# Performance work log

Hardware: AMD Instinct MI355X
Metric: run time of the kernel (lower is better)

The kernel has to match this reference:

```python
import jax, jax.numpy as jnp
import numpy as np

HEADS = 4
DIM_HEAD = 64
SCALE = 10.0
EPS = 1e-12  # matches torch F.normalize default eps


def setup_inputs() -> dict:
    key = jax.random.key(0)
    k1, k2, k3, k4, k5 = jax.random.split(key, 5)
    dim = 256
    hidden = HEADS * DIM_HEAD
    x = jax.random.normal(k1, (16, dim, 32, 32), dtype=jnp.float32)
    y = jax.random.normal(k2, (16, dim, 32, 32), dtype=jnp.float32)
    # 1x1 conv weights stored as 2D matrices (out_ch, in_ch)
    w_qkv = jax.random.normal(k3, (hidden * 3, dim), dtype=jnp.float32) * (1.0 / np.sqrt(dim))
    w_out = jax.random.normal(k4, (dim, hidden), dtype=jnp.float32) * (1.0 / np.sqrt(hidden))
    b_out = jax.random.normal(k5, (dim,), dtype=jnp.float32) * 0.01
    return {"x": x, "y": y, "w_qkv": w_qkv, "w_out": w_out, "b_out": b_out}


def _l2norm(t):
    # torch F.normalize(t, dim=-1): t / max(||t||_2, eps)
    n = jnp.sqrt(jnp.sum(t * t, axis=-1, keepdims=True))
    return t / jnp.maximum(n, EPS)


def reference(x, y, w_qkv, w_out, b_out):
    b, c, hh, ww = x.shape
    n_x = hh * ww
    n_y = y.shape[2] * y.shape[3]
    hidden = HEADS * DIM_HEAD

    # 1x1 convs == channel matmuls; only q from x and k,v from y are used
    w_q, w_k, w_v = w_qkv[:hidden], w_qkv[hidden:2 * hidden], w_qkv[2 * hidden:]
    q = jnp.einsum('oc,bcn->bon', w_q, x.reshape(b, c, n_x)).reshape(b, HEADS, DIM_HEAD, n_x)
    k = jnp.einsum('oc,bcn->bon', w_k, y.reshape(b, c, n_y)).reshape(b, HEADS, DIM_HEAD, n_y)
    v = jnp.einsum('oc,bcn->bon', w_v, y.reshape(b, c, n_y)).reshape(b, HEADS, DIM_HEAD, n_y)

    # l2norm over the spatial (last) axis, as in the source
    q = _l2norm(q)
    k = _l2norm(k)

    sim = jnp.einsum('bhdi,bhdj->bhij', q, k) * SCALE          # [b,h,n_x,n_y]
    attn = jax.nn.softmax(sim, axis=-1)
    out = jnp.einsum('bhij,bhdj->bhid', attn, v)                # [b,h,n_x,d]

    # 'b h (x y) d -> b (h d) x y'
    out = out.transpose(0, 1, 3, 2).reshape(b, hidden, hh, ww)
    out = jnp.einsum('oc,bcn->bon', w_out, out.reshape(b, hidden, n_x))
    out = out + b_out[None, :, None]
    return out.reshape(b, -1, hh, ww)
```

## Files before the change

### kernel.cpp

```cpp
#include <hip/hip_runtime.h>
#include <hip/hip_bf16.h>
#include <stdint.h>

typedef __attribute__((ext_vector_type(8))) short short8;
typedef __attribute__((ext_vector_type(4))) float f32x4;

#define MFMA16(a, b, c) __builtin_amdgcn_mfma_f32_16x16x32_bf16((a), (b), (c), 0, 0, 0)


__device__ __forceinline__ ushort f2bf(float f) {
  union { float f; unsigned u; } x; x.f = f;
  unsigned r = x.u + 0x7FFFu + ((x.u >> 16) & 1u);
  return (ushort)(r >> 16);
}

__device__ __forceinline__ float bf2f(ushort u) {
  union { unsigned u; float f; } x; x.u = ((unsigned)u) << 16;
  return x.f;
}

__device__ __forceinline__ short8 ld8(const ushort* p) {
  return *reinterpret_cast<const short8*>(p);
}

__device__ __forceinline__ void gll16(const void* g, void* l) {
  __builtin_amdgcn_global_load_lds(
      reinterpret_cast<const __attribute__((address_space(1))) unsigned int*>(
          reinterpret_cast<uintptr_t>(g)),
      reinterpret_cast<__attribute__((address_space(3))) unsigned int*>(
          reinterpret_cast<uintptr_t>(l)),
      16, 0, 0);
}

__global__ __launch_bounds__(256) void k_tcvt(const float* __restrict__ x,
    const float* __restrict__ y, ushort* __restrict__ xbt, ushort* __restrict__ ybt) {
  int tile = blockIdx.x;
  const float* src; ushort* dst;
  if (tile >= 1024) { tile -= 1024; src = y; dst = ybt; }
  else { src = x; dst = xbt; }
  int b = tile >> 6;
  int c0 = ((tile >> 4) & 3) << 6;
  int n0 = (tile & 15) << 6;
  __shared__ ushort lds[64][65];
  int tid = threadIdx.x;
  int nl = tid & 63, cl = tid >> 6;
  const float* sb = src + ((size_t)b << 18);
#pragma unroll
  for (int s = 0; s < 16; ++s) {
    int c = cl + (s << 2);
    lds[c][nl] = f2bf(sb[(size_t)(c0 + c) * 1024 + n0 + nl]);
  }
  __syncthreads();
  ushort* db = dst + ((size_t)b << 18);
  int cl2 = tid & 63, nl2 = tid >> 6;
#pragma unroll
  for (int s = 0; s < 16; ++s) {
    int n = nl2 + (s << 2);
    db[(size_t)(n0 + n) * 256 + c0 + cl2] = lds[cl2][n];
  }
}

__global__ __launch_bounds__(256) void k_wcvt(const float* __restrict__ wqkv,
    const float* __restrict__ wout, ushort* __restrict__ wqkvb, ushort* __restrict__ woutb) {
  const int total1 = 768 * 256;
  const int total = total1 + 256 * 256;
  for (int i = blockIdx.x * 256 + threadIdx.x; i < total; i += gridDim.x * 256) {
    if (i < total1) wqkvb[i] = f2bf(wqkv[i]);
    else woutb[i - total1] = f2bf(wout[i - total1]);
  }
}

__global__ __launch_bounds__(512, 6) void k_qkv(const ushort* __restrict__ wqkvb,
    const ushort* __restrict__ xbt, const ushort* __restrict__ ybt,
    ushort* __restrict__ qraw, ushort* __restrict__ kraw,
    ushort* __restrict__ vbuf, float* __restrict__ norms2) {
  int bid = blockIdx.x;
  int lid = (bid & 7) * 96 + (bid >> 3);
  int ox = lid % 24;
  int t = lid / 24;
  int nb = t & 1;
  int b = t >> 1;
  int o0 = ox * 32;
  const ushort* Bsrc = (o0 < 256) ? xbt : ybt;
  const ushort* Bm = Bsrc + ((size_t)b << 18);
  int tid = threadIdx.x;
  int l = tid & 63, w = tid >> 6;
  int r = l & 15, g = l >> 4;
  const ushort* Ab = wqkvb + (size_t)(o0 + r) * 256 + g * 8;
  const ushort* Bb = Bm + (size_t)(nb * 512 + w * 64 + r) * 256 + g * 8;
  f32x4 acc[2][4];
#pragma unroll
  for (int i = 0; i < 2; ++i)
#pragma unroll
    for (int j = 0; j < 4; ++j) acc[i][j] = (f32x4){0.f, 0.f, 0.f, 0.f};
#pragma unroll
  for (int ks = 0; ks < 8; ++ks) {
    short8 a0 = ld8(Ab + ks * 32);
    short8 a1 = ld8(Ab + 4096 + ks * 32);
#pragma unroll
    for (int nf = 0; nf < 4; ++nf) {
      short8 bv = ld8(Bb + (size_t)nf * 4096 + ks * 32);
      acc[0][nf] = MFMA16(a0, bv, acc[0][nf]);
      acc[1][nf] = MFMA16(a1, bv, acc[1][nf]);
    }
  }
  __shared__ float snorm[8][32];
  if (o0 < 512) {
    float ss[2][4];
#pragma unroll
    for (int mf = 0; mf < 2; ++mf)
#pragma unroll
      for (int reg = 0; reg < 4; ++reg) {
        float s = 0.f;
#pragma unroll
        for (int nf = 0; nf < 4; ++nf) { float v = acc[mf][nf][reg]; s += v * v; }
#pragma unroll
        for (int m = 1; m < 16; m <<= 1) s += __shfl_xor(s, m);
        ss[mf][reg] = s;
      }
    if (r == 0) {
#pragma unroll
      for (int mf = 0; mf < 2; ++mf)
#pragma unroll
        for (int reg = 0; reg < 4; ++reg)
          snorm[w][mf * 16 + g * 4 + reg] = ss[mf][reg];
    }
    __syncthreads();
    if (tid < 32) {
      float s = 0.f;
#pragma unroll
      for (int w2 = 0; w2 < 8; ++w2) s += snorm[w2][tid];
      norms2[(nb * 16 + b) * 512 + o0 + tid] = s;
    }
  }
#pragma unroll
  for (int mf = 0; mf < 2; ++mf) {
    int ob = o0 + mf * 16 + g * 4;
#pragma unroll
    for (int nf = 0; nf < 4; ++nf) {
      int n = nb * 512 + w * 64 + nf * 16 + r;
#pragma unroll
      for (int reg = 0; reg < 4; ++reg) {
        ushort v = f2bf(acc[mf][nf][reg]);
        int oo = ob + reg;
        if (o0 < 256)       qraw[(((size_t)b * 256 + oo) << 10) + n] = v;
        else if (o0 < 512)  kraw[(((size_t)b * 256 + (oo - 256)) << 10) + n] = v;
        else                vbuf[(((size_t)b * 256 + (oo - 512)) << 10) + n] = v;
      }
    }
  }
}

__global__ __launch_bounds__(256) void k_normt(const ushort* __restrict__ qraw,
    const ushort* __restrict__ kraw, const float* __restrict__ norms2,
    ushort* __restrict__ qt, ushort* __restrict__ kt) {
  int tile = blockIdx.x;
  const ushort* src; ushort* dst; int which;
  if (tile >= 1024) { tile -= 1024; src = kraw; dst = kt; which = 1; }
  else { src = qraw; dst = qt; which = 0; }
  int b = tile >> 6;
  int h = (tile >> 4) & 3;
  int n0 = (tile & 15) << 6;
  __shared__ ushort lds[64][65];
  __shared__ float fs[64];
  int tid = threadIdx.x;
  if (tid < 64) {
    int idx = b * 512 + which * 256 + h * 64 + tid;
    float ss = norms2[idx] + norms2[8192 + idx];
    fs[tid] = (which ? 1.0f : 10.0f) / fmaxf(sqrtf(ss), 1e-12f);
  }
  __syncthreads();
  const ushort* sb = src + (((size_t)b * 256 + h * 64) << 10);
  int nl = tid & 63, dl = tid >> 6;
#pragma unroll
  for (int s = 0; s < 16; ++s) {
    int d = dl + (s << 2);
    lds[d][nl] = f2bf(bf2f(sb[((size_t)d << 10) + n0 + nl]) * fs[d]);
  }
  __syncthreads();
  ushort* db = dst + (((size_t)(b * 4 + h) << 10) + n0) * 64;
  int dl2 = tid & 63, nl2 = tid >> 6;
#pragma unroll
  for (int s = 0; s < 16; ++s) {
    int n = nl2 + (s << 2);
    db[(size_t)n * 64 + dl2] = lds[dl2][n];
  }
}

__global__ __launch_bounds__(512, 2) void k_attn(const ushort* __restrict__ qt,
    const ushort* __restrict__ kt, const ushort* __restrict__ vbuf,
    ushort* __restrict__ aot) {
  int hb = blockIdx.x;
  int it = blockIdx.y;
  int h = hb & 3, b = hb >> 2;
  int tid = threadIdx.x;
  int l = tid & 63, w = tid >> 6;
  int r = l & 15, g = l >> 4;
  size_t ho = ((size_t)hb) << 16;
  const ushort* Q = qt + ho;
  const char* Kg = (const char*)(kt + ho);
  const char* Vg = (const char*)(vbuf + ((size_t)b << 18) + ((size_t)h << 16));
  int i0 = it * 256 + w * 32;

  __shared__ __align__(16) ushort Kb[2][4096];
  __shared__ __align__(16) ushort Vb[2][4096];
  __shared__ __align__(16) ushort plds[8][2048];

  int L = w * 1024 + l * 16;
  int srow = L >> 7;
  int swz = (srow & 7) << 4;
  int ksrc = L ^ swz;
  int vsrc_col = (L & 127) ^ swz;

  short8 qa[2][2];
#pragma unroll
  for (int mf = 0; mf < 2; ++mf)
#pragma unroll
    for (int ks = 0; ks < 2; ++ks)
      qa[mf][ks] = ld8(Q + (size_t)(i0 + mf * 16 + r) * 64 + ks * 32 + g * 8);

  f32x4 oacc[2][4];
  float rsum[2][4];
#pragma unroll
  for (int mf = 0; mf < 2; ++mf)
#pragma unroll
    for (int j = 0; j < 4; ++j) { oacc[mf][j] = (f32x4){0.f, 0.f, 0.f, 0.f}; rsum[mf][j] = 0.f; }

#define STAGE(buf, j0v) do { \
    gll16(Kg + (j0v) * 128 + ksrc, (char*)&Kb[buf][0] + w * 1024); \
    gll16(Vg + (size_t)srow * 2048 + (j0v) * 2 + vsrc_col, (char*)&Vb[buf][0] + w * 1024); \
  } while (0)

  STAGE(0, 0);
  __syncthreads();

  char* plc = (char*)plds[w];
  for (int t = 0; t < 16; ++t) {
    int cur = t & 1;
    if (t < 15) STAGE(cur ^ 1, (t + 1) * 64);
    const char* Kc = (const char*)&Kb[cur][0];
    const char* Vc = (const char*)&Vb[cur][0];
    f32x4 sacc[2][4];
#pragma unroll
    for (int mf = 0; mf < 2; ++mf)
#pragma unroll
      for (int nf = 0; nf < 4; ++nf) sacc[mf][nf] = (f32x4){0.f, 0.f, 0.f, 0.f};
#pragma unroll
    for (int nf = 0; nf < 4; ++nf) {
      int row = nf * 16 + r;
      int sw = (row & 7) << 4;
      short8 k0 = *reinterpret_cast<const short8*>(Kc + ((row * 128 + g * 16) ^ sw));
      short8 k1 = *reinterpret_cast<const short8*>(Kc + ((row * 128 + 64 + g * 16) ^ sw));
      sacc[0][nf] = MFMA16(qa[0][0], k0, sacc[0][nf]);
      sacc[0][nf] = MFMA16(qa[0][1], k1, sacc[0][nf]);
      sacc[1][nf] = MFMA16(qa[1][0], k0, sacc[1][nf]);
      sacc[1][nf] = MFMA16(qa[1][1], k1, sacc[1][nf]);
    }
#pragma unroll
    for (int mf = 0; mf < 2; ++mf)
#pragma unroll
      for (int nf = 0; nf < 4; ++nf)
#pragma unroll
        for (int reg = 0; reg < 4; ++reg) {
          float p = __expf(sacc[mf][nf][reg]);
          rsum[mf][reg] += p;
          union { float f; unsigned u; } cv; cv.f = p;
          int row = mf * 16 + g * 4 + reg;
          int xorv = ((row ^ (row >> 3)) & 7) << 4;
          int byteo = row * 128 + (((nf * 16 + r) * 2) ^ xorv);
          *(ushort*)(plc + byteo) = (ushort)(cv.u >> 16);
        }
    short8 pa[2][2];
#pragma unroll
    for (int mf = 0; mf < 2; ++mf)
#pragma unroll
      for (int ks = 0; ks < 2; ++ks) {
        int row = mf * 16 + r;
        int xorv = (row ^ (row >> 3)) & 7;
        int blk = (ks * 4 + g) ^ xorv;
        pa[mf][ks] = *reinterpret_cast<const short8*>(plc + row * 128 + blk * 16);
      }
#pragma unroll
    for (int df = 0; df < 4; ++df) {
      int row = df * 16 + r;
      int sw = (row & 7) << 4;
#pragma unroll
      for (int ks = 0; ks < 2; ++ks) {
        short8 vf = *reinterpret_cast<const short8*>(Vc + ((row * 128 + ks * 64 + g * 16) ^ sw));
        oacc[0][df] = MFMA16(pa[0][ks], vf, oacc[0][df]);
        oacc[1][df] = MFMA16(pa[1][ks], vf, oacc[1][df]);
      }
    }
    __syncthreads();
  }
#undef STAGE

#pragma unroll
  for (int mf = 0; mf < 2; ++mf)
#pragma unroll
    for (int reg = 0; reg < 4; ++reg) {
      float s = rsum[mf][reg];
#pragma unroll
      for (int m = 1; m < 16; m <<= 1) s += __shfl_xor(s, m);
      rsum[mf][reg] = 1.0f / s;
    }
#pragma unroll
  for (int mf = 0; mf < 2; ++mf)
#pragma unroll
    for (int df = 0; df < 4; ++df)
#pragma unroll
      for (int reg = 0; reg < 4; ++reg) {
        int i = i0 + mf * 16 + g * 4 + reg;
        int d = df * 16 + r;
        float vo = oacc[mf][df][reg] * rsum[mf][reg];
        aot[((size_t)b << 18) + (size_t)i * 256 + h * 64 + d] = f2bf(vo);
      }
}

__global__ __launch_bounds__(512, 6) void k_out(const ushort* __restrict__ woutb,
    const ushort* __restrict__ aot, const float* __restrict__ bout,
    float* __restrict__ out) {
  int bid = blockIdx.x;
  int lid = (bid & 7) * 64 + (bid >> 3);
  int ox = lid & 15;
  int t = lid >> 4;
  int nb = t & 1;
  int b = t >> 1;
  int o0 = ox * 16;
  int tid = threadIdx.x, l = tid & 63, w = tid >> 6, r = l & 15, g = l >> 4;
  const ushort* Ab = woutb + (size_t)(o0 + r) * 256 + g * 8;
  const ushort* Bb = aot + ((size_t)b << 18) + (size_t)(nb * 512 + w * 64 + r) * 256 + g * 8;
  f32x4 acc[4];
#pragma unroll
  for (int j = 0; j < 4; ++j) acc[j] = (f32x4){0.f, 0.f, 0.f, 0.f};
#pragma unroll
  for (int ks = 0; ks < 8; ++ks) {
    short8 a0 = ld8(Ab + ks * 32);
#pragma unroll
    for (int nf = 0; nf < 4; ++nf) {
      short8 bv = ld8(Bb + (size_t)nf * 4096 + ks * 32);
      acc[nf] = MFMA16(a0, bv, acc[nf]);
    }
  }
  float bias[4];
#pragma unroll
  for (int reg = 0; reg < 4; ++reg) bias[reg] = bout[o0 + g * 4 + reg];
#pragma unroll
  for (int nf = 0; nf < 4; ++nf)
#pragma unroll
    for (int reg = 0; reg < 4; ++reg) {
      size_t o = (size_t)(b * 256 + o0 + g * 4 + reg);
      out[(o << 10) + nb * 512 + w * 64 + nf * 16 + r] = acc[nf][reg] + bias[reg];
    }
}

extern "C" void kernel_launch(void* const* d_in, const int* in_sizes, int n_in,
                              void* d_out, int out_size, void* d_ws, size_t ws_size,
                              hipStream_t stream) {
  const float* x     = (const float*)d_in[0];
  const float* y     = (const float*)d_in[1];
  const float* wqkv  = (const float*)d_in[2];
  const float* wout  = (const float*)d_in[3];
  const float* bout  = (const float*)d_in[4];
  float* out = (float*)d_out;
  char* ws = (char*)d_ws;

  ushort* xbt   = (ushort*)(ws + 0ull);
  ushort* qt    = (ushort*)(ws + 0ull);
  ushort* ybt   = (ushort*)(ws + 8388608ull);
  ushort* kt    = (ushort*)(ws + 8388608ull);
  ushort* qraw  = (ushort*)(ws + 16777216ull);
  ushort* aot   = (ushort*)(ws + 16777216ull);
  ushort* kraw  = (ushort*)(ws + 25165824ull);
  ushort* vbuf  = (ushort*)(ws + 33554432ull);
  ushort* wqkvb = (ushort*)(ws + 41943040ull);
  ushort* woutb = (ushort*)(ws + 42336256ull);
  float*  norms2= (float*) (ws + 42467328ull);

  k_tcvt<<<2048, 256, 0, stream>>>(x, y, xbt, ybt);
  k_wcvt<<<256, 256, 0, stream>>>(wqkv, wout, wqkvb, woutb);
  k_qkv<<<768, 512, 0, stream>>>(wqkvb, xbt, ybt, qraw, kraw, vbuf, norms2);
  k_normt<<<2048, 256, 0, stream>>>(qraw, kraw, norms2, qt, kt);
  k_attn<<<dim3(64, 4), 512, 0, stream>>>(qt, kt, vbuf, aot);
  k_out<<<512, 512, 0, stream>>>(woutb, aot, bout, out);
}
```

Before: 186.8 us.

## Fuse normalization into QKV GEMM, merge weight conversion, and halve attention tile

```diff
diff --git a/kernel.cpp b/kernel.cpp
--- a/kernel.cpp
+++ b/kernel.cpp
@@ -4,6 +4,7 @@
 
 typedef __attribute__((ext_vector_type(8))) short short8;
 typedef __attribute__((ext_vector_type(4))) float f32x4;
+typedef __attribute__((ext_vector_type(4))) unsigned short ushort4v;
 
 #define MFMA16(a, b, c) __builtin_amdgcn_mfma_f32_16x16x32_bf16((a), (b), (c), 0, 0, 0)
 
@@ -12,11 +13,6 @@
   union { float f; unsigned u; } x; x.f = f;
   unsigned r = x.u + 0x7FFFu + ((x.u >> 16) & 1u);
   return (ushort)(r >> 16);
-}
-
-__device__ __forceinline__ float bf2f(ushort u) {
-  union { unsigned u; float f; } x; x.u = ((unsigned)u) << 16;
-  return x.f;
 }
 
 __device__ __forceinline__ short8 ld8(const ushort* p) {
@@ -33,8 +29,19 @@
 }
 
 __global__ __launch_bounds__(256) void k_tcvt(const float* __restrict__ x,
-    const float* __restrict__ y, ushort* __restrict__ xbt, ushort* __restrict__ ybt) {
+    const float* __restrict__ y, ushort* __restrict__ xbt, ushort* __restrict__ ybt,
+    const float* __restrict__ wqkv, const float* __restrict__ wout,
+    ushort* __restrict__ wqkvb, ushort* __restrict__ woutb) {
   int tile = blockIdx.x;
+  if (tile >= 2048) {
+    const int total1 = 768 * 256;
+    const int total = total1 + 256 * 256;
+    for (int i = (tile - 2048) * 256 + threadIdx.x; i < total; i += 64 * 256) {
+      if (i < total1) wqkvb[i] = f2bf(wqkv[i]);
+      else woutb[i - total1] = f2bf(wout[i - total1]);
+    }
+    return;
+  }
   const float* src; ushort* dst;
   if (tile >= 1024) { tile -= 1024; src = y; dst = ybt; }
   else { src = x; dst = xbt; }
@@ -60,26 +67,13 @@
   }
 }
 
-__global__ __launch_bounds__(256) void k_wcvt(const float* __restrict__ wqkv,
-    const float* __restrict__ wout, ushort* __restrict__ wqkvb, ushort* __restrict__ woutb) {
-  const int total1 = 768 * 256;
-  const int total = total1 + 256 * 256;
-  for (int i = blockIdx.x * 256 + threadIdx.x; i < total; i += gridDim.x * 256) {
-    if (i < total1) wqkvb[i] = f2bf(wqkv[i]);
-    else woutb[i - total1] = f2bf(wout[i - total1]);
-  }
-}
-
-__global__ __launch_bounds__(512, 6) void k_qkv(const ushort* __restrict__ wqkvb,
+__global__ __launch_bounds__(512, 4) void k_qkv(const ushort* __restrict__ wqkvb,
     const ushort* __restrict__ xbt, const ushort* __restrict__ ybt,
-    ushort* __restrict__ qraw, ushort* __restrict__ kraw,
-    ushort* __restrict__ vbuf, float* __restrict__ norms2) {
+    ushort* __restrict__ qt, ushort* __restrict__ kt, ushort* __restrict__ vbuf) {
   int bid = blockIdx.x;
-  int lid = (bid & 7) * 96 + (bid >> 3);
+  int lid = (bid & 7) * 48 + (bid >> 3);
   int ox = lid % 24;
-  int t = lid / 24;
-  int nb = t & 1;
-  int b = t >> 1;
+  int b = lid / 24;
   int o0 = ox * 32;
   const ushort* Bsrc = (o0 < 256) ? xbt : ybt;
   const ushort* Bm = Bsrc + ((size_t)b << 18);
@@ -87,25 +81,26 @@
   int l = tid & 63, w = tid >> 6;
   int r = l & 15, g = l >> 4;
   const ushort* Ab = wqkvb + (size_t)(o0 + r) * 256 + g * 8;
-  const ushort* Bb = Bm + (size_t)(nb * 512 + w * 64 + r) * 256 + g * 8;
-  f32x4 acc[2][4];
+  const ushort* Bb = Bm + (size_t)(w * 128 + r) * 256 + g * 8;
+  f32x4 acc[2][8];
 #pragma unroll
   for (int i = 0; i < 2; ++i)
 #pragma unroll
-    for (int j = 0; j < 4; ++j) acc[i][j] = (f32x4){0.f, 0.f, 0.f, 0.f};
+    for (int j = 0; j < 8; ++j) acc[i][j] = (f32x4){0.f, 0.f, 0.f, 0.f};
 #pragma unroll
   for (int ks = 0; ks < 8; ++ks) {
     short8 a0 = ld8(Ab + ks * 32);
     short8 a1 = ld8(Ab + 4096 + ks * 32);
 #pragma unroll
-    for (int nf = 0; nf < 4; ++nf) {
+    for (int nf = 0; nf < 8; ++nf) {
       short8 bv = ld8(Bb + (size_t)nf * 4096 + ks * 32);
       acc[0][nf] = MFMA16(a0, bv, acc[0][nf]);
       acc[1][nf] = MFMA16(a1, bv, acc[1][nf]);
     }
   }
-  __shared__ float snorm[8][32];
   if (o0 < 512) {
+    __shared__ float snorm[8][32];
+    __shared__ float fs[32];
     float ss[2][4];
 #pragma unroll
     for (int mf = 0; mf < 2; ++mf)
@@ -113,7 +108,7 @@
       for (int reg = 0; reg < 4; ++reg) {
         float s = 0.f;
 #pragma unroll
-        for (int nf = 0; nf < 4; ++nf) { float v = acc[mf][nf][reg]; s += v * v; }
+        for (int nf = 0; nf < 8; ++nf) { float v = acc[mf][nf][reg]; s += v * v; }
 #pragma unroll
         for (int m = 1; m < 16; m <<= 1) s += __shfl_xor(s, m);
         ss[mf][reg] = s;
@@ -130,64 +125,43 @@
       float s = 0.f;
 #pragma unroll
       for (int w2 = 0; w2 < 8; ++w2) s += snorm[w2][tid];
-      norms2[(nb * 16 + b) * 512 + o0 + tid] = s;
-    }
-  }
-#pragma unroll
-  for (int mf = 0; mf < 2; ++mf) {
-    int ob = o0 + mf * 16 + g * 4;
-#pragma unroll
-    for (int nf = 0; nf < 4; ++nf) {
-      int n = nb * 512 + w * 64 + nf * 16 + r;
-#pragma unroll
-      for (int reg = 0; reg < 4; ++reg) {
-        ushort v = f2bf(acc[mf][nf][reg]);
-        int oo = ob + reg;
-        if (o0 < 256)       qraw[(((size_t)b * 256 + oo) << 10) + n] = v;
-        else if (o0 < 512)  kraw[(((size_t)b * 256 + (oo - 256)) << 10) + n] = v;
-        else                vbuf[(((size_t)b * 256 + (oo - 512)) << 10) + n] = v;
-      }
-    }
-  }
-}
-
-__global__ __launch_bounds__(256) void k_normt(const ushort* __restrict__ qraw,
-    const ushort* __restrict__ kraw, const float* __restrict__ norms2,
-    ushort* __restrict__ qt, ushort* __restrict__ kt) {
-  int tile = blockIdx.x;
-  const ushort* src; ushort* dst; int which;
-  if (tile >= 1024) { tile -= 1024; src = kraw; dst = kt; which = 1; }
-  else { src = qraw; dst = qt; which = 0; }
-  int b = tile >> 6;
-  int h = (tile >> 4) & 3;
-  int n0 = (tile & 15) << 6;
-  __shared__ ushort lds[64][65];
-  __shared__ float fs[64];
-  int tid = threadIdx.x;
-  if (tid < 64) {
-    int idx = b * 512 + which * 256 + h * 64 + tid;
-    float ss = norms2[idx] + norms2[8192 + idx];
-    fs[tid] = (which ? 1.0f : 10.0f) / fmaxf(sqrtf(ss), 1e-12f);
-  }
-  __syncthreads();
-  const ushort* sb = src + (((size_t)b * 256 + h * 64) << 10);
-  int nl = tid & 63, dl = tid >> 6;
-#pragma unroll
-  for (int s = 0; s < 16; ++s) {
-    int d = dl + (s << 2);
-    lds[d][nl] = f2bf(bf2f(sb[((size_t)d << 10) + n0 + nl]) * fs[d]);
-  }
-  __syncthreads();
-  ushort* db = dst + (((size_t)(b * 4 + h) << 10) + n0) * 64;
-  int dl2 = tid & 63, nl2 = tid >> 6;
-#pragma unroll
-  for (int s = 0; s < 16; ++s) {
-    int n = nl2 + (s << 2);
-    db[(size_t)n * 64 + dl2] = lds[dl2][n];
-  }
-}
-
-__global__ __launch_bounds__(512, 2) void k_attn(const ushort* __restrict__ qt,
+      fs[tid] = ((o0 < 256) ? 10.0f : 1.0f) / fmaxf(sqrtf(s), 1e-12f);
+    }
+    __syncthreads();
+    float fr[2][4];
+#pragma unroll
+    for (int mf = 0; mf < 2; ++mf)
+#pragma unroll
+      for (int reg = 0; reg < 4; ++reg) fr[mf][reg] = fs[mf * 16 + g * 4 + reg];
+    int od = (o0 < 256) ? o0 : o0 - 256;
+    int hh = od >> 6, d0 = od & 63;
+    ushort* dst = ((o0 < 256) ? qt : kt) + (((size_t)(b * 4 + hh)) << 16);
+#pragma unroll
+    for (int mf = 0; mf < 2; ++mf)
+#pragma unroll
+      for (int nf = 0; nf < 8; ++nf) {
+        int n = w * 128 + nf * 16 + r;
+        ushort4v u;
+#pragma unroll
+        for (int reg = 0; reg < 4; ++reg) u[reg] = f2bf(acc[mf][nf][reg] * fr[mf][reg]);
+        *reinterpret_cast<ushort4v*>(dst + (size_t)n * 64 + d0 + mf * 16 + g * 4) = u;
+      }
+  } else {
+#pragma unroll
+    for (int mf = 0; mf < 2; ++mf) {
+      int ob = o0 - 512 + mf * 16 + g * 4;
+#pragma unroll
+      for (int nf = 0; nf < 8; ++nf) {
+        int n = w * 128 + nf * 16 + r;
+#pragma unroll
+        for (int reg = 0; reg < 4; ++reg)
+          vbuf[(((size_t)b * 256 + ob + reg) << 10) + n] = f2bf(acc[mf][nf][reg]);
+      }
+    }
+  }
+}
+
+__global__ __launch_bounds__(512, 4) void k_attn(const ushort* __restrict__ qt,
     const ushort* __restrict__ kt, const ushort* __restrict__ vbuf,
     ushort* __restrict__ aot) {
   int hb = blockIdx.x;
@@ -200,11 +174,11 @@
   const ushort* Q = qt + ho;
   const char* Kg = (const char*)(kt + ho);
   const char* Vg = (const char*)(vbuf + ((size_t)b << 18) + ((size_t)h << 16));
-  int i0 = it * 256 + w * 32;
+  int i0 = it * 128 + w * 16;
 
   __shared__ __align__(16) ushort Kb[2][4096];
   __shared__ __align__(16) ushort Vb[2][4096];
-  __shared__ __align__(16) ushort plds[8][2048];
+  __shared__ __align__(16) ushort plds[8][1024];
 
   int L = w * 1024 + l * 16;
   int srow = L >> 7;
@@ -212,19 +186,15 @@
   int ksrc = L ^ swz;
   int vsrc_col = (L & 127) ^ swz;
 
-  short8 qa[2][2];
-#pragma unroll
-  for (int mf = 0; mf < 2; ++mf)
-#pragma unroll
-    for (int ks = 0; ks < 2; ++ks)
-      qa[mf][ks] = ld8(Q + (size_t)(i0 + mf * 16 + r) * 64 + ks * 32 + g * 8);
-
-  f32x4 oacc[2][4];
-  float rsum[2][4];
-#pragma unroll
-  for (int mf = 0; mf < 2; ++mf)
-#pragma unroll
-    for (int j = 0; j < 4; ++j) { oacc[mf][j] = (f32x4){0.f, 0.f, 0.f, 0.f}; rsum[mf][j] = 0.f; }
+  short8 qa[2];
+#pragma unroll
+  for (int ks = 0; ks < 2; ++ks)
+    qa[ks] = ld8(Q + (size_t)(i0 + r) * 64 + ks * 32 + g * 8);
+
+  f32x4 oacc[4];
+  float rsum[4];
+#pragma unroll
+  for (int j = 0; j < 4; ++j) { oacc[j] = (f32x4){0.f, 0.f, 0.f, 0.f}; rsum[j] = 0.f; }
 
 #define STAGE(buf, j0v) do { \
     gll16(Kg + (j0v) * 128 + ksrc, (char*)&Kb[buf][0] + w * 1024); \
@@ -240,46 +210,37 @@
     if (t < 15) STAGE(cur ^ 1, (t + 1) * 64);
     const char* Kc = (const char*)&Kb[cur][0];
     const char* Vc = (const char*)&Vb[cur][0];
-    f32x4 sacc[2][4];
-#pragma unroll
-    for (int mf = 0; mf < 2; ++mf)
-#pragma unroll
-      for (int nf = 0; nf < 4; ++nf) sacc[mf][nf] = (f32x4){0.f, 0.f, 0.f, 0.f};
+    f32x4 sacc[4];
+#pragma unroll
+    for (int nf = 0; nf < 4; ++nf) sacc[nf] = (f32x4){0.f, 0.f, 0.f, 0.f};
 #pragma unroll
     for (int nf = 0; nf < 4; ++nf) {
       int row = nf * 16 + r;
       int sw = (row & 7) << 4;
       short8 k0 = *reinterpret_cast<const short8*>(Kc + ((row * 128 + g * 16) ^ sw));
       short8 k1 = *reinterpret_cast<const short8*>(Kc + ((row * 128 + 64 + g * 16) ^ sw));
-      sacc[0][nf] = MFMA16(qa[0][0], k0, sacc[0][nf]);
-      sacc[0][nf] = MFMA16(qa[0][1], k1, sacc[0][nf]);
-      sacc[1][nf] = MFMA16(qa[1][0], k0, sacc[1][nf]);
-      sacc[1][nf] = MFMA16(qa[1][1], k1, sacc[1][nf]);
-    }
-#pragma unroll
-    for (int mf = 0; mf < 2; ++mf)
-#pragma unroll
-      for (int nf = 0; nf < 4; ++nf)
-#pragma unroll
-        for (int reg = 0; reg < 4; ++reg) {
-          float p = __expf(sacc[mf][nf][reg]);
-          rsum[mf][reg] += p;
-          union { float f; unsigned u; } cv; cv.f = p;
-          int row = mf * 16 + g * 4 + reg;
-          int xorv = ((row ^ (row >> 3)) & 7) << 4;
-          int byteo = row * 128 + (((nf * 16 + r) * 2) ^ xorv);
-          *(ushort*)(plc + byteo) = (ushort)(cv.u >> 16);
-        }
-    short8 pa[2][2];
-#pragma unroll
-    for (int mf = 0; mf < 2; ++mf)
-#pragma unroll
-      for (int ks = 0; ks < 2; ++ks) {
-        int row = mf * 16 + r;
-        int xorv = (row ^ (row >> 3)) & 7;
-        int blk = (ks * 4 + g) ^ xorv;
-        pa[mf][ks] = *reinterpret_cast<const short8*>(plc + row * 128 + blk * 16);
-      }
+      sacc[nf] = MFMA16(qa[0], k0, sacc[nf]);
+      sacc[nf] = MFMA16(qa[1], k1, sacc[nf]);
+    }
+#pragma unroll
+    for (int nf = 0; nf < 4; ++nf)
+#pragma unroll
+      for (int reg = 0; reg < 4; ++reg) {
+        float p = __expf(sacc[nf][reg]);
+        rsum[reg] += p;
+        union { float f; unsigned u; } cv; cv.f = p;
+        int row = g * 4 + reg;
+        int xorv = ((row ^ (row >> 3)) & 7) << 4;
+        int byteo = row * 128 + (((nf * 16 + r) * 2) ^ xorv);
+        *(ushort*)(plc + byteo) = (ushort)(cv.u >> 16);
+      }
+    short8 pa[2];
+#pragma unroll
+    for (int ks = 0; ks < 2; ++ks) {
+      int xorv = (r ^ (r >> 3)) & 7;
+      int blk = (ks * 4 + g) ^ xorv;
+      pa[ks] = *reinterpret_cast<const short8*>(plc + r * 128 + blk * 16);
+    }
 #pragma unroll
     for (int df = 0; df < 4; ++df) {
       int row = df * 16 + r;
@@ -287,8 +248,7 @@
 #pragma unroll
       for (int ks = 0; ks < 2; ++ks) {
         short8 vf = *reinterpret_cast<const short8*>(Vc + ((row * 128 + ks * 64 + g * 16) ^ sw));
-        oacc[0][df] = MFMA16(pa[0][ks], vf, oacc[0][df]);
-        oacc[1][df] = MFMA16(pa[1][ks], vf, oacc[1][df]);
+        oacc[df] = MFMA16(pa[ks], vf, oacc[df]);
       }
     }
     __syncthreads();
@@ -296,25 +256,21 @@
 #undef STAGE
 
 #pragma unroll
-  for (int mf = 0; mf < 2; ++mf)
+  for (int reg = 0; reg < 4; ++reg) {
+    float s = rsum[reg];
+#pragma unroll
+    for (int m = 1; m < 16; m <<= 1) s += __shfl_xor(s, m);
+    rsum[reg] = 1.0f / s;
+  }
+#pragma unroll
+  for (int df = 0; df < 4; ++df)
 #pragma unroll
     for (int reg = 0; reg < 4; ++reg) {
-      float s = rsum[mf][reg];
-#pragma unroll
-      for (int m = 1; m < 16; m <<= 1) s += __shfl_xor(s, m);
-      rsum[mf][reg] = 1.0f / s;
-    }
-#pragma unroll
-  for (int mf = 0; mf < 2; ++mf)
-#pragma unroll
-    for (int df = 0; df < 4; ++df)
-#pragma unroll
-      for (int reg = 0; reg < 4; ++reg) {
-        int i = i0 + mf * 16 + g * 4 + reg;
-        int d = df * 16 + r;
-        float vo = oacc[mf][df][reg] * rsum[mf][reg];
-        aot[((size_t)b << 18) + (size_t)i * 256 + h * 64 + d] = f2bf(vo);
-      }
+      int i = i0 + g * 4 + reg;
+      int d = df * 16 + r;
+      float vo = oacc[df][reg] * rsum[reg];
+      aot[((size_t)b << 18) + (size_t)i * 256 + h * 64 + d] = f2bf(vo);
+    }
 }
 
 __global__ __launch_bounds__(512, 6) void k_out(const ushort* __restrict__ woutb,
@@ -366,21 +322,16 @@
   char* ws = (char*)d_ws;
 
   ushort* xbt   = (ushort*)(ws + 0ull);
-  ushort* qt    = (ushort*)(ws + 0ull);
+  ushort* aot   = (ushort*)(ws + 0ull);
   ushort* ybt   = (ushort*)(ws + 8388608ull);
-  ushort* kt    = (ushort*)(ws + 8388608ull);
-  ushort* qraw  = (ushort*)(ws + 16777216ull);
-  ushort* aot   = (ushort*)(ws + 16777216ull);
-  ushort* kraw  = (ushort*)(ws + 25165824ull);
+  ushort* qt    = (ushort*)(ws + 16777216ull);
+  ushort* kt    = (ushort*)(ws + 25165824ull);
   ushort* vbuf  = (ushort*)(ws + 33554432ull);
   ushort* wqkvb = (ushort*)(ws + 41943040ull);
   ushort* woutb = (ushort*)(ws + 42336256ull);
-  float*  norms2= (float*) (ws + 42467328ull);
-
-  k_tcvt<<<2048, 256, 0, stream>>>(x, y, xbt, ybt);
-  k_wcvt<<<256, 256, 0, stream>>>(wqkv, wout, wqkvb, woutb);
-  k_qkv<<<768, 512, 0, stream>>>(wqkvb, xbt, ybt, qraw, kraw, vbuf, norms2);
-  k_normt<<<2048, 256, 0, stream>>>(qraw, kraw, norms2, qt, kt);
-  k_attn<<<dim3(64, 4), 512, 0, stream>>>(qt, kt, vbuf, aot);
+
+  k_tcvt<<<2112, 256, 0, stream>>>(x, y, xbt, ybt, wqkv, wout, wqkvb, woutb);
+  k_qkv<<<384, 512, 0, stream>>>(wqkvb, xbt, ybt, qt, kt, vbuf);
+  k_attn<<<dim3(64, 8), 512, 0, stream>>>(qt, kt, vbuf, aot);
   k_out<<<512, 512, 0, stream>>>(woutb, aot, bout, out);
 }
```

New measurement: 186.3 us. Within noise of the previous version (-0.3%).
